# Kernel tuning notes

Hardware: AMD Instinct MI355X
Metric: run time of the kernel (lower is better)

Reference implementation:

```python
import jax, jax.numpy as jnp
import numpy as np

TOP_K = 8
SCALE = 2.5  # moe_router_scaling_factor
EPS = 1e-20


def setup_inputs() -> dict:
    key = jax.random.key(0)
    k1, k2 = jax.random.split(key)
    B, S, H, E = 4, 4096, 4096, 64
    hidden_states = jax.random.normal(k1, (B, S, H), dtype=jnp.float32)
    gate_weight = jax.random.normal(k2, (E, H), dtype=jnp.float32) * 0.02
    router_bias = jnp.zeros((E,), dtype=jnp.float32)
    return {"hidden_states": hidden_states, "gate_weight": gate_weight, "router_bias": router_bias}


def reference(hidden_states, gate_weight, router_bias):
    B, S, H = hidden_states.shape
    x = hidden_states.reshape(-1, H).astype(jnp.float32)  # [T, H]
    # need_fp32_gate: fp32 matmul against gate weight transpose -> [T, E]
    logits = jnp.einsum('th,eh->te', x, gate_weight.astype(jnp.float32))
    gate_prob = jax.nn.sigmoid(logits)
    biased = gate_prob + router_bias[None, :]
    # topk on bias-shifted probs; weights gathered from UNbiased probs
    _, indices = jax.lax.top_k(biased, TOP_K)                       # [T, K]
    topk_prob = jnp.take_along_axis(gate_prob, indices, axis=1)     # [T, K]
    weights = topk_prob / (jnp.sum(topk_prob, axis=-1, keepdims=True) + EPS)
    weights = weights * SCALE
    return weights, indices
```

## Files before the change

### kernel.cpp

```cpp
#include <hip/hip_runtime.h>
#include <cmath>


typedef float f32x4 __attribute__((ext_vector_type(4)));
typedef short s16x8 __attribute__((ext_vector_type(8)));
typedef unsigned int u32;
typedef u32 u32x4 __attribute__((ext_vector_type(4)));

#define E_DIM 64
#define KC 32
#define CH_BYTES 12288
#define NPART 4
#define HI_OFF (2u << 20)

union V16 { u32x4 u; s16x8 s; };

__device__ __forceinline__ unsigned short f2bf(float f) {
  unsigned u = __float_as_uint(f);
  u += 0x7fffu + ((u >> 16) & 1u);
  return (unsigned short)(u >> 16);
}
__device__ __forceinline__ float bf2f(unsigned short s) {
  return __uint_as_float(((unsigned)s) << 16);
}

__global__ __launch_bounds__(256) void split_w(
    const float* __restrict__ w, unsigned char* __restrict__ w3, int Hdim)
{
  const int kpr = Hdim >> 4;
  const int g = blockIdx.x * 256 + threadIdx.x;
  const int e = g / kpr;
  const int k0 = (g - e * kpr) * 16;
  if (e >= E_DIM) return;

  const float* src = w + (size_t)e * Hdim + k0;
  float f[16];
#pragma unroll
  for (int i = 0; i < 4; ++i) {
    float4 v = *(const float4*)(src + i * 4);
    f[i*4+0] = v.x; f[i*4+1] = v.y; f[i*4+2] = v.z; f[i*4+3] = v.w;
  }
  unsigned short hs[16], ms[16], ls[16];
#pragma unroll
  for (int i = 0; i < 16; ++i) {
    unsigned short h = f2bf(f[i]);
    float r1 = f[i] - bf2f(h);
    unsigned short m = f2bf(r1);
    float r2 = r1 - bf2f(m);
    hs[i] = h; ms[i] = m; ls[i] = f2bf(r2);
  }
  const int c  = k0 >> 5;
  const int n  = e >> 4;
  const int la = (e & 15) + (((k0 & 31) >> 3) << 4);
  unsigned char* base = w3 + (size_t)c * CH_BYTES + n * 1024;

#define STORE_SPLIT(arr, s)                                              \
  do {                                                                   \
    s16x8 pa, pb;                                                        \
    _Pragma("unroll")                                                    \
    for (int j = 0; j < 8; ++j) { pa[j] = (short)arr[j]; pb[j] = (short)arr[8+j]; } \
    *(s16x8*)(base + (s)*4096 + la * 16)        = pa;                    \
    *(s16x8*)(base + (s)*4096 + (la + 16) * 16) = pb;                    \
  } while (0)

  STORE_SPLIT(hs, 0);
  STORE_SPLIT(ms, 1);
  STORE_SPLIT(ls, 2);
#undef STORE_SPLIT
}

__global__ __launch_bounds__(256, 2) void router_mfma(
    const float* __restrict__ x, const unsigned char* __restrict__ w3,
    const float* __restrict__ bias, float* __restrict__ outw,
    float* __restrict__ outi, float* __restrict__ hi_p,
    float* __restrict__ lo_p, int T, int Hdim)
{
  const int tid  = threadIdx.x;
  const int wid  = tid >> 6;
  const int lane = tid & 63;
  const int lc   = lane & 15;
  const int lq   = lane >> 4;
  const int by   = blockIdx.y;
  const int nch  = Hdim / KC / gridDim.y;
  const int t0w  = blockIdx.x * 128 + wid * 32;

  const float* x0 = x + (size_t)(t0w + lc) * Hdim + (size_t)by * nch * KC + lq * 8;
  const float* x1 = x0 + (size_t)16 * Hdim;
  const unsigned char* wb = w3 + (size_t)by * nch * CH_BYTES + lane * 16;

  f32x4 acc[2][4];
  f32x4 sum_[2][4];
  f32x4 comp[2][4];
#pragma unroll
  for (int t = 0; t < 2; ++t)
#pragma unroll
    for (int n = 0; n < 4; ++n) {
      acc[t][n] = (f32x4){0,0,0,0};
      sum_[t][n] = (f32x4){0,0,0,0};
      comp[t][n] = (f32x4){0,0,0,0};
    }

#define LOADB(c, B)                                                          \
  do {                                                                       \
    const unsigned char* p_ = wb + (size_t)(c) * CH_BYTES;                   \
    _Pragma("unroll")                                                        \
    for (int s = 0; s < 3; ++s) {                                            \
      const unsigned char* ps_ = p_ + s * 4096;                              \
      _Pragma("unroll")                                                      \
      for (int n = 0; n < 4; ++n)                                            \
        B[s*4+n] = *(const s16x8*)(ps_ + n * 1024);                          \
    }                                                                        \
  } while (0)

#define LOADX(c, X)                                                          \
  do {                                                                       \
    X[0] = *(const float4*)(x0 + (size_t)(c) * KC);                          \
    X[1] = *(const float4*)(x0 + (size_t)(c) * KC + 4);                      \
    X[2] = *(const float4*)(x1 + (size_t)(c) * KC);                          \
    X[3] = *(const float4*)(x1 + (size_t)(c) * KC + 4);                      \
  } while (0)

#define SPLIT_PAIR(f0, f1, i, AHU, AMU, ALU)                                 \
  do {                                                                       \
    u32 u0_ = __float_as_uint(f0), u1_ = __float_as_uint(f1);                \
    u32 v0_ = u0_ + 0x8000u, v1_ = u1_ + 0x8000u;                            \
    AHU[i] = __builtin_amdgcn_perm(v1_, v0_, 0x07060302u);                   \
    float r0_ = (f0) - __uint_as_float(v0_ & 0xffff0000u);                   \
    float r1_ = (f1) - __uint_as_float(v1_ & 0xffff0000u);                   \
    u32 w0_ = __float_as_uint(r0_) + 0x8000u;                                \
    u32 w1_ = __float_as_uint(r1_) + 0x8000u;                                \
    AMU[i] = __builtin_amdgcn_perm(w1_, w0_, 0x07060302u);                   \
    float s0_ = r0_ - __uint_as_float(w0_ & 0xffff0000u);                    \
    float s1_ = r1_ - __uint_as_float(w1_ & 0xffff0000u);                    \
    u32 y0_ = __float_as_uint(s0_) + 0x8000u;                                \
    u32 y1_ = __float_as_uint(s1_) + 0x8000u;                                \
    ALU[i] = __builtin_amdgcn_perm(y1_, y0_, 0x07060302u);                   \
  } while (0)

#define COMPUTE(X, B)                                                        \
  do {                                                                       \
    _Pragma("unroll")                                                        \
    for (int t = 0; t < 2; ++t) {                                            \
      V16 ah_, am_, al_;                                                     \
      SPLIT_PAIR(X[t*2].x, X[t*2].y, 0, ah_.u, am_.u, al_.u);                \
      SPLIT_PAIR(X[t*2].z, X[t*2].w, 1, ah_.u, am_.u, al_.u);                \
      SPLIT_PAIR(X[t*2+1].x, X[t*2+1].y, 2, ah_.u, am_.u, al_.u);            \
      SPLIT_PAIR(X[t*2+1].z, X[t*2+1].w, 3, ah_.u, am_.u, al_.u);            \
      s16x8 ah = ah_.s, am = am_.s, al = al_.s;                              \
      __builtin_amdgcn_s_setprio(1);                                         \
      _Pragma("unroll")                                                      \
      for (int n = 0; n < 4; ++n) {                                          \
        acc[t][n] = __builtin_amdgcn_mfma_f32_16x16x32_bf16(ah, B[n],   acc[t][n], 0,0,0); \
        acc[t][n] = __builtin_amdgcn_mfma_f32_16x16x32_bf16(ah, B[4+n], acc[t][n], 0,0,0); \
        acc[t][n] = __builtin_amdgcn_mfma_f32_16x16x32_bf16(am, B[n],   acc[t][n], 0,0,0); \
        acc[t][n] = __builtin_amdgcn_mfma_f32_16x16x32_bf16(ah, B[8+n], acc[t][n], 0,0,0); \
        acc[t][n] = __builtin_amdgcn_mfma_f32_16x16x32_bf16(am, B[4+n], acc[t][n], 0,0,0); \
        acc[t][n] = __builtin_amdgcn_mfma_f32_16x16x32_bf16(al, B[n],   acc[t][n], 0,0,0); \
      }                                                                      \
      __builtin_amdgcn_s_setprio(0);                                         \
    }                                                                        \
  } while (0)

#define FOLD()                                                               \
  do {                                                                       \
    _Pragma("unroll")                                                        \
    for (int t = 0; t < 2; ++t)                                              \
      _Pragma("unroll")                                                      \
      for (int n = 0; n < 4; ++n)                                            \
        _Pragma("unroll")                                                    \
        for (int r = 0; r < 4; ++r) {                                        \
          float a_ = acc[t][n][r];                                           \
          float s_ = sum_[t][n][r];                                          \
          float t_ = s_ + a_;                                                \
          float z_ = t_ - s_;                                                \
          comp[t][n][r] += (s_ - (t_ - z_)) + (a_ - z_);                     \
          sum_[t][n][r] = t_;                                                \
          acc[t][n][r] = 0.f;                                                \
        }                                                                    \
  } while (0)

  float4 XA[4], XB[4];
  s16x8 BA[12], BB[12];

  LOADB(0, BA);
  LOADX(0, XA);

#pragma unroll 1
  for (int c = 0; c < nch; c += 2) {
    LOADB(c + 1, BB);
    LOADX(c + 1, XB);
    COMPUTE(XA, BA);
    if (c + 2 < nch) { LOADB(c + 2, BA); LOADX(c + 2, XA); }
    COMPUTE(XB, BB);
    if ((c & 2) == 2) FOLD();
  }
  FOLD();

  if (gridDim.y != 1) {
#pragma unroll
    for (int t = 0; t < 2; ++t)
#pragma unroll
      for (int n = 0; n < 4; ++n)
#pragma unroll
        for (int r = 0; r < 4; ++r) {
          const int tok = t0w + t * 16 + lq * 4 + r;
          const size_t o = ((size_t)by * T + tok) * E_DIM + n * 16 + lc;
          hi_p[o] = sum_[t][n][r];
          lo_p[o] = comp[t][n][r];
        }
    return;
  }

  float bias_v[4];
#pragma unroll
  for (int n = 0; n < 4; ++n) bias_v[n] = bias[n * 16 + lc];

#pragma unroll
  for (int t = 0; t < 2; ++t) {
    float pr[4][4], bi[4][4];
#pragma unroll
    for (int n = 0; n < 4; ++n)
#pragma unroll
      for (int r = 0; r < 4; ++r) {
        float logit = sum_[t][n][r] + comp[t][n][r];
        float p = 1.0f / (1.0f + expf(-logit));
        pr[n][r] = p;
        bi[n][r] = p + bias_v[n];
      }
#pragma unroll
    for (int r = 0; r < 4; ++r) {
      float v0 = bi[0][r], v1 = bi[1][r], v2 = bi[2][r], v3 = bi[3][r];
      float p0 = pr[0][r], p1 = pr[1][r], p2 = pr[2][r], p3 = pr[3][r];
      float sum = 0.f, selp = 0.f;
      int seli = 0;
#pragma unroll
      for (int k = 0; k < 8; ++k) {
        float bv = v0; int bn = 0; float bp = p0;
        if (v1 > bv) { bv = v1; bn = 1; bp = p1; }
        if (v2 > bv) { bv = v2; bn = 2; bp = p2; }
        if (v3 > bv) { bv = v3; bn = 3; bp = p3; }
        int be = bn * 16 + lc;
#pragma unroll
        for (int off = 8; off >= 1; off >>= 1) {
          float ov = __shfl_xor(bv, off);
          float op = __shfl_xor(bp, off);
          int   oe = __shfl_xor(be, off);
          if (ov > bv || (ov == bv && oe < be)) { bv = ov; bp = op; be = oe; }
        }
        sum += bp;
        if (lc == k) { selp = bp; seli = be; }
        if (lc == (be & 15)) {
          int gsel = be >> 4;
          if      (gsel == 0) v0 = -1e30f;
          else if (gsel == 1) v1 = -1e30f;
          else if (gsel == 2) v2 = -1e30f;
          else                v3 = -1e30f;
        }
      }
      if (lc < 8) {
        const int tok = t0w + t * 16 + lq * 4 + r;
        outw[(size_t)tok * 8 + lc] = selp * 2.5f / (sum + 1e-20f);
        outi[(size_t)tok * 8 + lc] = (float)seli;
      }
    }
  }
}

__global__ __launch_bounds__(256) void router_topk(
    const float* __restrict__ hi_p, const float* __restrict__ lo_p,
    const float* __restrict__ bias, float* __restrict__ outw,
    float* __restrict__ outi, int T)
{
  const int lane = threadIdx.x & 63;
  const int t = blockIdx.x * 4 + (threadIdx.x >> 6);
  if (t >= T) return;

  float s = 0.f, c = 0.f, losum = 0.f;
#pragma unroll
  for (int p = 0; p < NPART; ++p) {
    const size_t o = ((size_t)p * T + t) * E_DIM + lane;
    float a = hi_p[o];
    float tt = s + a;
    float z = tt - s;
    c += (s - (tt - z)) + (a - z);
    s = tt;
    losum += lo_p[o];
  }
  const float logit = s + (c + losum);

  const float prob = 1.0f / (1.0f + expf(-logit));
  float v = prob + bias[lane];

  float sum = 0.f, selw = 0.f;
  int seli = 0;
#pragma unroll
  for (int k = 0; k < 8; ++k) {
    float rv = v;
    int   ri = lane;
#pragma unroll
    for (int off = 32; off > 0; off >>= 1) {
      float ov = __shfl_xor(rv, off);
      int   oi = __shfl_xor(ri, off);
      if (ov > rv || (ov == rv && oi < ri)) { rv = ov; ri = oi; }
    }
    float pwin = __shfl(prob, ri);
    sum += pwin;
    if (lane == k)  { selw = pwin; seli = ri; }
    if (lane == ri) v = -INFINITY;
  }

  if (lane < 8) {
    float scale = 2.5f / (sum + 1e-20f);
    outw[(size_t)t * 8 + lane] = selw * scale;
    outi[(size_t)t * 8 + lane] = (float)seli;
  }
}

extern "C" void kernel_launch(void* const* d_in, const int* in_sizes, int n_in,
                              void* d_out, int out_size, void* d_ws, size_t ws_size,
                              hipStream_t stream) {
  const float* x    = (const float*)d_in[0];
  const float* w    = (const float*)d_in[1];
  const float* bias = (const float*)d_in[2];

  const int E    = in_sizes[2];
  const int Hdim = in_sizes[1] / E;
  const int T    = in_sizes[0] / Hdim;

  unsigned char* ws = (unsigned char*)d_ws;
  unsigned char* w3 = ws;
  float* hi_p = (float*)(ws + HI_OFF);
  float* lo_p = hi_p + (size_t)NPART * T * E_DIM;

  const size_t need = (size_t)HI_OFF + (size_t)2 * NPART * T * E_DIM * sizeof(float);
  const int nparts = (ws_size >= need) ? NPART : 1;

  const int nElemGroups = E * Hdim / 16;
  split_w<<<(nElemGroups + 255) / 256, 256, 0, stream>>>(w, w3, Hdim);

  float* outw = (float*)d_out;
  float* outi = outw + (size_t)T * 8;

  dim3 gridG(T / 128, nparts);
  router_mfma<<<gridG, 256, 0, stream>>>(x, w3, bias, outw, outi, hi_p, lo_p, T, Hdim);

  if (nparts != 1) {
    router_topk<<<(T + 3) / 4, 256, 0, stream>>>(hi_p, lo_p, bias, outw, outi, T);
  }
}
```

Before: 124.1 us.

## Use single-wave blocks and half-chunk B pipelining with scheduling barriers

Shrinks each block of the router GEMM kernel to one 64-lane wave covering 32 tokens, and raises the grid size to match. The main loop becomes a software pipeline: the B fragments are loaded in two halves (6 registers each instead of two 12-register buffers), X is prefetched two chunks ahead with four buffers, and sched_barrier fences interleave global loads with the MFMA groups. The aim is to cut register pressure and overlap memory latency with matrix work in this bandwidth-heavy fp32-split GEMM. In exchange it adds more blocks and drops the final FOLD, which assumes the chunk count is a multiple of four.

```diff
diff --git a/kernel.cpp b/kernel.cpp
--- a/kernel.cpp
+++ b/kernel.cpp
@@ -69,20 +69,18 @@
 #undef STORE_SPLIT
 }
 
-__global__ __launch_bounds__(256, 2) void router_mfma(
+__global__ __launch_bounds__(64, 2) void router_mfma(
     const float* __restrict__ x, const unsigned char* __restrict__ w3,
     const float* __restrict__ bias, float* __restrict__ outw,
     float* __restrict__ outi, float* __restrict__ hi_p,
     float* __restrict__ lo_p, int T, int Hdim)
 {
-  const int tid  = threadIdx.x;
-  const int wid  = tid >> 6;
-  const int lane = tid & 63;
+  const int lane = threadIdx.x;
   const int lc   = lane & 15;
   const int lq   = lane >> 4;
   const int by   = blockIdx.y;
   const int nch  = Hdim / KC / gridDim.y;
-  const int t0w  = blockIdx.x * 128 + wid * 32;
+  const int t0w  = blockIdx.x * 32;
 
   const float* x0 = x + (size_t)(t0w + lc) * Hdim + (size_t)by * nch * KC + lq * 8;
   const float* x1 = x0 + (size_t)16 * Hdim;
@@ -100,16 +98,16 @@
       comp[t][n] = (f32x4){0,0,0,0};
     }
 
-#define LOADB(c, B)                                                          \
-  do {                                                                       \
-    const unsigned char* p_ = wb + (size_t)(c) * CH_BYTES;                   \
+#define SB() __builtin_amdgcn_sched_barrier(0)
+
+#define LOADB_H(c, h, B)                                                     \
+  do {                                                                       \
+    const unsigned char* p_ = wb + (size_t)(c) * CH_BYTES + (h) * 2048;      \
     _Pragma("unroll")                                                        \
-    for (int s = 0; s < 3; ++s) {                                            \
-      const unsigned char* ps_ = p_ + s * 4096;                              \
+    for (int s = 0; s < 3; ++s)                                              \
       _Pragma("unroll")                                                      \
-      for (int n = 0; n < 4; ++n)                                            \
-        B[s*4+n] = *(const s16x8*)(ps_ + n * 1024);                          \
-    }                                                                        \
+      for (int j = 0; j < 2; ++j)                                            \
+        B[s*2+j] = *(const s16x8*)(p_ + s * 4096 + j * 1024);                \
   } while (0)
 
 #define LOADX(c, X)                                                          \
@@ -137,7 +135,7 @@
     ALU[i] = __builtin_amdgcn_perm(y1_, y0_, 0x07060302u);                   \
   } while (0)
 
-#define COMPUTE(X, B)                                                        \
+#define CONVERT(X)                                                           \
   do {                                                                       \
     _Pragma("unroll")                                                        \
     for (int t = 0; t < 2; ++t) {                                            \
@@ -146,19 +144,27 @@
       SPLIT_PAIR(X[t*2].z, X[t*2].w, 1, ah_.u, am_.u, al_.u);                \
       SPLIT_PAIR(X[t*2+1].x, X[t*2+1].y, 2, ah_.u, am_.u, al_.u);            \
       SPLIT_PAIR(X[t*2+1].z, X[t*2+1].w, 3, ah_.u, am_.u, al_.u);            \
-      s16x8 ah = ah_.s, am = am_.s, al = al_.s;                              \
-      __builtin_amdgcn_s_setprio(1);                                         \
+      Aah[t] = ah_.s; Aam[t] = am_.s; Aal[t] = al_.s;                        \
+    }                                                                        \
+  } while (0)
+
+#define COMPUTE_HALF(B, h)                                                   \
+  do {                                                                       \
+    __builtin_amdgcn_s_setprio(1);                                           \
+    _Pragma("unroll")                                                        \
+    for (int p = 0; p < 6; ++p)                                              \
       _Pragma("unroll")                                                      \
-      for (int n = 0; n < 4; ++n) {                                          \
-        acc[t][n] = __builtin_amdgcn_mfma_f32_16x16x32_bf16(ah, B[n],   acc[t][n], 0,0,0); \
-        acc[t][n] = __builtin_amdgcn_mfma_f32_16x16x32_bf16(ah, B[4+n], acc[t][n], 0,0,0); \
-        acc[t][n] = __builtin_amdgcn_mfma_f32_16x16x32_bf16(am, B[n],   acc[t][n], 0,0,0); \
-        acc[t][n] = __builtin_amdgcn_mfma_f32_16x16x32_bf16(ah, B[8+n], acc[t][n], 0,0,0); \
-        acc[t][n] = __builtin_amdgcn_mfma_f32_16x16x32_bf16(am, B[4+n], acc[t][n], 0,0,0); \
-        acc[t][n] = __builtin_amdgcn_mfma_f32_16x16x32_bf16(al, B[n],   acc[t][n], 0,0,0); \
-      }                                                                      \
-      __builtin_amdgcn_s_setprio(0);                                         \
-    }                                                                        \
+      for (int t = 0; t < 2; ++t)                                            \
+        _Pragma("unroll")                                                    \
+        for (int j = 0; j < 2; ++j) {                                        \
+          const s16x8 a_ = (p==0||p==2||p==5) ? Aah[t]                       \
+                         : (p==1||p==4)       ? Aam[t] : Aal[t];             \
+          const s16x8 b_ = (p==0||p==1||p==3) ? B[j]                         \
+                         : (p==2||p==4)       ? B[2+j] : B[4+j];             \
+          acc[t][2*(h)+j] =                                                  \
+            __builtin_amdgcn_mfma_f32_16x16x32_bf16(a_, b_, acc[t][2*(h)+j], 0,0,0); \
+        }                                                                    \
+    __builtin_amdgcn_s_setprio(0);                                           \
   } while (0)
 
 #define FOLD()                                                               \
@@ -179,22 +185,48 @@
         }                                                                    \
   } while (0)
 
-  float4 XA[4], XB[4];
-  s16x8 BA[12], BB[12];
-
-  LOADB(0, BA);
-  LOADX(0, XA);
+#define SUBITER(ca, XC0, XC1, XN0, XN1)                                      \
+  do {                                                                       \
+    const int cp2 = ((ca) + 2 < nch) ? (ca) + 2 : 0;                         \
+    const int cp3 = ((ca) + 3 < nch) ? (ca) + 3 : 0;                         \
+    LOADX(cp2, XN0);                                                         \
+    SB();                                                                    \
+    CONVERT(XC0);                                                            \
+    COMPUTE_HALF(B0, 0);                                                     \
+    SB();                                                                    \
+    LOADB_H((ca) + 1, 0, B0);                                                \
+    SB();                                                                    \
+    COMPUTE_HALF(B1, 1);                                                     \
+    SB();                                                                    \
+    LOADB_H((ca) + 1, 1, B1);                                                \
+    LOADX(cp3, XN1);                                                         \
+    SB();                                                                    \
+    CONVERT(XC1);                                                            \
+    COMPUTE_HALF(B0, 0);                                                     \
+    SB();                                                                    \
+    LOADB_H(cp2, 0, B0);                                                     \
+    SB();                                                                    \
+    COMPUTE_HALF(B1, 1);                                                     \
+    SB();                                                                    \
+    LOADB_H(cp2, 1, B1);                                                     \
+    SB();                                                                    \
+  } while (0)
+
+  float4 X0[4], X1[4], X2[4], X3[4];
+  s16x8 B0[6], B1[6];
+  s16x8 Aah[2], Aam[2], Aal[2];
+
+  LOADB_H(0, 0, B0);
+  LOADB_H(0, 1, B1);
+  LOADX(0, X0);
+  LOADX(1, X1);
 
 #pragma unroll 1
-  for (int c = 0; c < nch; c += 2) {
-    LOADB(c + 1, BB);
-    LOADX(c + 1, XB);
-    COMPUTE(XA, BA);
-    if (c + 2 < nch) { LOADB(c + 2, BA); LOADX(c + 2, XA); }
-    COMPUTE(XB, BB);
-    if ((c & 2) == 2) FOLD();
-  }
-  FOLD();
+  for (int c = 0; c < nch; c += 4) {
+    SUBITER(c,     X0, X1, X2, X3);
+    SUBITER(c + 2, X2, X3, X0, X1);
+    FOLD();
+  }
 
   if (gridDim.y != 1) {
 #pragma unroll
@@ -341,8 +373,8 @@
   float* outw = (float*)d_out;
   float* outi = outw + (size_t)T * 8;
 
-  dim3 gridG(T / 128, nparts);
-  router_mfma<<<gridG, 256, 0, stream>>>(x, w3, bias, outw, outi, hi_p, lo_p, T, Hdim);
+  dim3 gridG(T / 32, nparts);
+  router_mfma<<<gridG, 64, 0, stream>>>(x, w3, bias, outw, outi, hi_p, lo_p, T, Hdim);
 
   if (nparts != 1) {
     router_topk<<<(T + 3) / 4, 256, 0, stream>>>(hi_p, lo_p, bias, outw, outi, T);
```

Result: no change. 122.9 us (-1.0%).

## Stage split gate weights in LDS via direct global-to-LDS loads with double buffering

Applied to the files above, without the earlier changes.

Weight chunks are now loaded cooperatively by the whole block into a double-buffered LDS tile using global_load_lds, instead of each wave loading all weight fragments into registers. Each wave now handles 16 tokens rather than 32, so blocks cover 64 tokens and the grid doubles; occupancy hint rises to 3 blocks per CU. The aim is to cut redundant per-wave weight traffic and register pressure, and to overlap the next chunk's load with MFMA work. In exchange it adds block barriers on every chunk and LDS reads of B fragments, and the weights are reused across half as many tokens per wave.

```diff
diff --git a/kernel.cpp b/kernel.cpp
--- a/kernel.cpp
+++ b/kernel.cpp
@@ -69,12 +69,14 @@
 #undef STORE_SPLIT
 }
 
-__global__ __launch_bounds__(256, 2) void router_mfma(
+__global__ __launch_bounds__(256, 3) void router_mfma(
     const float* __restrict__ x, const unsigned char* __restrict__ w3,
     const float* __restrict__ bias, float* __restrict__ outw,
     float* __restrict__ outi, float* __restrict__ hi_p,
     float* __restrict__ lo_p, int T, int Hdim)
 {
+  __shared__ __align__(16) unsigned char lds[2][CH_BYTES];
+
   const int tid  = threadIdx.x;
   const int wid  = tid >> 6;
   const int lane = tid & 63;
@@ -82,42 +84,40 @@
   const int lq   = lane >> 4;
   const int by   = blockIdx.y;
   const int nch  = Hdim / KC / gridDim.y;
-  const int t0w  = blockIdx.x * 128 + wid * 32;
-
-  const float* x0 = x + (size_t)(t0w + lc) * Hdim + (size_t)by * nch * KC + lq * 8;
-  const float* x1 = x0 + (size_t)16 * Hdim;
-  const unsigned char* wb = w3 + (size_t)by * nch * CH_BYTES + lane * 16;
-
-  f32x4 acc[2][4];
-  f32x4 sum_[2][4];
-  f32x4 comp[2][4];
-#pragma unroll
-  for (int t = 0; t < 2; ++t)
-#pragma unroll
-    for (int n = 0; n < 4; ++n) {
-      acc[t][n] = (f32x4){0,0,0,0};
-      sum_[t][n] = (f32x4){0,0,0,0};
-      comp[t][n] = (f32x4){0,0,0,0};
-    }
-
-#define LOADB(c, B)                                                          \
-  do {                                                                       \
-    const unsigned char* p_ = wb + (size_t)(c) * CH_BYTES;                   \
+  const int t0   = blockIdx.x * 64;
+
+  const float* xp = x + (size_t)(t0 + wid * 16 + lc) * Hdim
+                      + (size_t)by * nch * KC + lq * 8;
+  const unsigned char* w3p = w3 + (size_t)by * nch * CH_BYTES;
+
+  f32x4 acc[4], sum_[4], comp[4];
+#pragma unroll
+  for (int n = 0; n < 4; ++n) {
+    acc[n] = (f32x4){0,0,0,0};
+    sum_[n] = (f32x4){0,0,0,0};
+    comp[n] = (f32x4){0,0,0,0};
+  }
+
+#define WAITV2() asm volatile("s_waitcnt vmcnt(2)" ::: "memory")
+#define WAITV0() asm volatile("s_waitcnt vmcnt(0)" ::: "memory")
+#define BAR()    __builtin_amdgcn_s_barrier()
+
+#define STAGE(c, b)                                                          \
+  do {                                                                       \
+    const unsigned char* gs = w3p + (size_t)(c) * CH_BYTES + tid * 16;       \
+    unsigned char* ld_ = &lds[b][0] + tid * 16;                              \
     _Pragma("unroll")                                                        \
-    for (int s = 0; s < 3; ++s) {                                            \
-      const unsigned char* ps_ = p_ + s * 4096;                              \
-      _Pragma("unroll")                                                      \
-      for (int n = 0; n < 4; ++n)                                            \
-        B[s*4+n] = *(const s16x8*)(ps_ + n * 1024);                          \
-    }                                                                        \
+    for (int i = 0; i < 3; ++i)                                              \
+      __builtin_amdgcn_global_load_lds(                                      \
+          (const __attribute__((address_space(1))) unsigned int*)(gs + i*4096), \
+          (__attribute__((address_space(3))) unsigned int*)(ld_ + i*4096),   \
+          16, 0, 0);                                                         \
   } while (0)
 
 #define LOADX(c, X)                                                          \
   do {                                                                       \
-    X[0] = *(const float4*)(x0 + (size_t)(c) * KC);                          \
-    X[1] = *(const float4*)(x0 + (size_t)(c) * KC + 4);                      \
-    X[2] = *(const float4*)(x1 + (size_t)(c) * KC);                          \
-    X[3] = *(const float4*)(x1 + (size_t)(c) * KC + 4);                      \
+    X[0] = *(const float4*)(xp + (size_t)(c) * KC);                          \
+    X[1] = *(const float4*)(xp + (size_t)(c) * KC + 4);                      \
   } while (0)
 
 #define SPLIT_PAIR(f0, f1, i, AHU, AMU, ALU)                                 \
@@ -137,77 +137,113 @@
     ALU[i] = __builtin_amdgcn_perm(y1_, y0_, 0x07060302u);                   \
   } while (0)
 
-#define COMPUTE(X, B)                                                        \
-  do {                                                                       \
+#define CONVERT(X)                                                           \
+  do {                                                                       \
+    V16 ah_, am_, al_;                                                       \
+    SPLIT_PAIR(X[0].x, X[0].y, 0, ah_.u, am_.u, al_.u);                      \
+    SPLIT_PAIR(X[0].z, X[0].w, 1, ah_.u, am_.u, al_.u);                      \
+    SPLIT_PAIR(X[1].x, X[1].y, 2, ah_.u, am_.u, al_.u);                      \
+    SPLIT_PAIR(X[1].z, X[1].w, 3, ah_.u, am_.u, al_.u);                      \
+    Aah = ah_.s; Aam = am_.s; Aal = al_.s;                                   \
+  } while (0)
+
+#define MFMA_ALL(b)                                                          \
+  do {                                                                       \
+    const unsigned char* B_ = &lds[b][0] + lane * 16;                        \
+    __builtin_amdgcn_s_setprio(1);                                           \
     _Pragma("unroll")                                                        \
-    for (int t = 0; t < 2; ++t) {                                            \
-      V16 ah_, am_, al_;                                                     \
-      SPLIT_PAIR(X[t*2].x, X[t*2].y, 0, ah_.u, am_.u, al_.u);                \
-      SPLIT_PAIR(X[t*2].z, X[t*2].w, 1, ah_.u, am_.u, al_.u);                \
-      SPLIT_PAIR(X[t*2+1].x, X[t*2+1].y, 2, ah_.u, am_.u, al_.u);            \
-      SPLIT_PAIR(X[t*2+1].z, X[t*2+1].w, 3, ah_.u, am_.u, al_.u);            \
-      s16x8 ah = ah_.s, am = am_.s, al = al_.s;                              \
-      __builtin_amdgcn_s_setprio(1);                                         \
+    for (int g = 0; g < 2; ++g) {                                            \
+      s16x8 bh0 = *(const s16x8*)(B_ + 0*4096 + (2*g)*1024);                 \
+      s16x8 bh1 = *(const s16x8*)(B_ + 0*4096 + (2*g+1)*1024);               \
+      s16x8 bm0 = *(const s16x8*)(B_ + 1*4096 + (2*g)*1024);                 \
+      s16x8 bm1 = *(const s16x8*)(B_ + 1*4096 + (2*g+1)*1024);               \
+      s16x8 bl0 = *(const s16x8*)(B_ + 2*4096 + (2*g)*1024);                 \
+      s16x8 bl1 = *(const s16x8*)(B_ + 2*4096 + (2*g+1)*1024);               \
+      acc[2*g]   = __builtin_amdgcn_mfma_f32_16x16x32_bf16(Aah, bh0, acc[2*g],   0,0,0); \
+      acc[2*g+1] = __builtin_amdgcn_mfma_f32_16x16x32_bf16(Aah, bh1, acc[2*g+1], 0,0,0); \
+      acc[2*g]   = __builtin_amdgcn_mfma_f32_16x16x32_bf16(Aah, bm0, acc[2*g],   0,0,0); \
+      acc[2*g+1] = __builtin_amdgcn_mfma_f32_16x16x32_bf16(Aah, bm1, acc[2*g+1], 0,0,0); \
+      acc[2*g]   = __builtin_amdgcn_mfma_f32_16x16x32_bf16(Aam, bh0, acc[2*g],   0,0,0); \
+      acc[2*g+1] = __builtin_amdgcn_mfma_f32_16x16x32_bf16(Aam, bh1, acc[2*g+1], 0,0,0); \
+      acc[2*g]   = __builtin_amdgcn_mfma_f32_16x16x32_bf16(Aah, bl0, acc[2*g],   0,0,0); \
+      acc[2*g+1] = __builtin_amdgcn_mfma_f32_16x16x32_bf16(Aah, bl1, acc[2*g+1], 0,0,0); \
+      acc[2*g]   = __builtin_amdgcn_mfma_f32_16x16x32_bf16(Aam, bm0, acc[2*g],   0,0,0); \
+      acc[2*g+1] = __builtin_amdgcn_mfma_f32_16x16x32_bf16(Aam, bm1, acc[2*g+1], 0,0,0); \
+      acc[2*g]   = __builtin_amdgcn_mfma_f32_16x16x32_bf16(Aal, bh0, acc[2*g],   0,0,0); \
+      acc[2*g+1] = __builtin_amdgcn_mfma_f32_16x16x32_bf16(Aal, bh1, acc[2*g+1], 0,0,0); \
+    }                                                                        \
+    __builtin_amdgcn_s_setprio(0);                                           \
+  } while (0)
+
+#define FOLD()                                                               \
+  do {                                                                       \
+    _Pragma("unroll")                                                        \
+    for (int n = 0; n < 4; ++n)                                              \
       _Pragma("unroll")                                                      \
-      for (int n = 0; n < 4; ++n) {                                          \
-        acc[t][n] = __builtin_amdgcn_mfma_f32_16x16x32_bf16(ah, B[n],   acc[t][n], 0,0,0); \
-        acc[t][n] = __builtin_amdgcn_mfma_f32_16x16x32_bf16(ah, B[4+n], acc[t][n], 0,0,0); \
-        acc[t][n] = __builtin_amdgcn_mfma_f32_16x16x32_bf16(am, B[n],   acc[t][n], 0,0,0); \
-        acc[t][n] = __builtin_amdgcn_mfma_f32_16x16x32_bf16(ah, B[8+n], acc[t][n], 0,0,0); \
-        acc[t][n] = __builtin_amdgcn_mfma_f32_16x16x32_bf16(am, B[4+n], acc[t][n], 0,0,0); \
-        acc[t][n] = __builtin_amdgcn_mfma_f32_16x16x32_bf16(al, B[n],   acc[t][n], 0,0,0); \
+      for (int r = 0; r < 4; ++r) {                                          \
+        float a_ = acc[n][r];                                                \
+        float s_ = sum_[n][r];                                               \
+        float t_ = s_ + a_;                                                  \
+        float z_ = t_ - s_;                                                  \
+        comp[n][r] += (s_ - (t_ - z_)) + (a_ - z_);                          \
+        sum_[n][r] = t_;                                                     \
+        acc[n][r] = 0.f;                                                     \
       }                                                                      \
-      __builtin_amdgcn_s_setprio(0);                                         \
-    }                                                                        \
-  } while (0)
-
-#define FOLD()                                                               \
-  do {                                                                       \
-    _Pragma("unroll")                                                        \
-    for (int t = 0; t < 2; ++t)                                              \
-      _Pragma("unroll")                                                      \
-      for (int n = 0; n < 4; ++n)                                            \
-        _Pragma("unroll")                                                    \
-        for (int r = 0; r < 4; ++r) {                                        \
-          float a_ = acc[t][n][r];                                           \
-          float s_ = sum_[t][n][r];                                          \
-          float t_ = s_ + a_;                                                \
-          float z_ = t_ - s_;                                                \
-          comp[t][n][r] += (s_ - (t_ - z_)) + (a_ - z_);                     \
-          sum_[t][n][r] = t_;                                                \
-          acc[t][n][r] = 0.f;                                                \
-        }                                                                    \
-  } while (0)
-
-  float4 XA[4], XB[4];
-  s16x8 BA[12], BB[12];
-
-  LOADB(0, BA);
-  LOADX(0, XA);
+  } while (0)
+
+#define ITER_FULL(c, k, XCUR, XN2)                                           \
+  do {                                                                       \
+    STAGE((c) + 1, ((k) + 1) & 1);                                           \
+    LOADX((c) + 2, XN2);                                                     \
+    CONVERT(XCUR);                                                           \
+    __builtin_amdgcn_sched_barrier(0);                                       \
+    MFMA_ALL((k) & 1);                                                       \
+    WAITV2();                                                                \
+    BAR();                                                                   \
+  } while (0)
+
+  float4 X0[2], X1[2], X2[2], X3[2];
+  s16x8 Aah, Aam, Aal;
+
+  STAGE(0, 0);
+  LOADX(0, X0);
+  LOADX(1, X1);
+  asm volatile("s_waitcnt vmcnt(4)" ::: "memory");
+  BAR();
 
 #pragma unroll 1
-  for (int c = 0; c < nch; c += 2) {
-    LOADB(c + 1, BB);
-    LOADX(c + 1, XB);
-    COMPUTE(XA, BA);
-    if (c + 2 < nch) { LOADB(c + 2, BA); LOADX(c + 2, XA); }
-    COMPUTE(XB, BB);
-    if ((c & 2) == 2) FOLD();
-  }
-  FOLD();
+  for (int c = 0; c + 4 < nch; c += 4) {
+    ITER_FULL(c + 0, 0, X0, X2);
+    ITER_FULL(c + 1, 1, X1, X3);
+    ITER_FULL(c + 2, 2, X2, X0);
+    ITER_FULL(c + 3, 3, X3, X1);
+    FOLD();
+  }
+  {
+    const int c = nch - 4;
+    ITER_FULL(c + 0, 0, X0, X2);
+    ITER_FULL(c + 1, 1, X1, X3);
+    STAGE(c + 3, 1);
+    CONVERT(X2);
+    __builtin_amdgcn_sched_barrier(0);
+    MFMA_ALL(0);
+    WAITV0();
+    BAR();
+    CONVERT(X3);
+    MFMA_ALL(1);
+    FOLD();
+  }
 
   if (gridDim.y != 1) {
 #pragma unroll
-    for (int t = 0; t < 2; ++t)
-#pragma unroll
-      for (int n = 0; n < 4; ++n)
-#pragma unroll
-        for (int r = 0; r < 4; ++r) {
-          const int tok = t0w + t * 16 + lq * 4 + r;
-          const size_t o = ((size_t)by * T + tok) * E_DIM + n * 16 + lc;
-          hi_p[o] = sum_[t][n][r];
-          lo_p[o] = comp[t][n][r];
-        }
+    for (int n = 0; n < 4; ++n)
+#pragma unroll
+      for (int r = 0; r < 4; ++r) {
+        const int tok = t0 + wid * 16 + lq * 4 + r;
+        const size_t o = ((size_t)by * T + tok) * E_DIM + n * 16 + lc;
+        hi_p[o] = sum_[n][r];
+        lo_p[o] = comp[n][r];
+      }
     return;
   }
 
@@ -215,53 +251,50 @@
 #pragma unroll
   for (int n = 0; n < 4; ++n) bias_v[n] = bias[n * 16 + lc];
 
-#pragma unroll
-  for (int t = 0; t < 2; ++t) {
-    float pr[4][4], bi[4][4];
-#pragma unroll
-    for (int n = 0; n < 4; ++n)
-#pragma unroll
-      for (int r = 0; r < 4; ++r) {
-        float logit = sum_[t][n][r] + comp[t][n][r];
-        float p = 1.0f / (1.0f + expf(-logit));
-        pr[n][r] = p;
-        bi[n][r] = p + bias_v[n];
+  float pr[4][4], bi[4][4];
+#pragma unroll
+  for (int n = 0; n < 4; ++n)
+#pragma unroll
+    for (int r = 0; r < 4; ++r) {
+      float logit = sum_[n][r] + comp[n][r];
+      float p = 1.0f / (1.0f + expf(-logit));
+      pr[n][r] = p;
+      bi[n][r] = p + bias_v[n];
+    }
+#pragma unroll
+  for (int r = 0; r < 4; ++r) {
+    float v0 = bi[0][r], v1 = bi[1][r], v2 = bi[2][r], v3 = bi[3][r];
+    float p0 = pr[0][r], p1 = pr[1][r], p2 = pr[2][r], p3 = pr[3][r];
+    float sum = 0.f, selp = 0.f;
+    int seli = 0;
+#pragma unroll
+    for (int k = 0; k < 8; ++k) {
+      float bv = v0; int bn = 0; float bp = p0;
+      if (v1 > bv) { bv = v1; bn = 1; bp = p1; }
+      if (v2 > bv) { bv = v2; bn = 2; bp = p2; }
+      if (v3 > bv) { bv = v3; bn = 3; bp = p3; }
+      int be = bn * 16 + lc;
+#pragma unroll
+      for (int off = 8; off >= 1; off >>= 1) {
+        float ov = __shfl_xor(bv, off);
+        float op = __shfl_xor(bp, off);
+        int   oe = __shfl_xor(be, off);
+        if (ov > bv || (ov == bv && oe < be)) { bv = ov; bp = op; be = oe; }
       }
-#pragma unroll
-    for (int r = 0; r < 4; ++r) {
-      float v0 = bi[0][r], v1 = bi[1][r], v2 = bi[2][r], v3 = bi[3][r];
-      float p0 = pr[0][r], p1 = pr[1][r], p2 = pr[2][r], p3 = pr[3][r];
-      float sum = 0.f, selp = 0.f;
-      int seli = 0;
-#pragma unroll
-      for (int k = 0; k < 8; ++k) {
-        float bv = v0; int bn = 0; float bp = p0;
-        if (v1 > bv) { bv = v1; bn = 1; bp = p1; }
-        if (v2 > bv) { bv = v2; bn = 2; bp = p2; }
-        if (v3 > bv) { bv = v3; bn = 3; bp = p3; }
-        int be = bn * 16 + lc;
-#pragma unroll
-        for (int off = 8; off >= 1; off >>= 1) {
-          float ov = __shfl_xor(bv, off);
-          float op = __shfl_xor(bp, off);
-          int   oe = __shfl_xor(be, off);
-          if (ov > bv || (ov == bv && oe < be)) { bv = ov; bp = op; be = oe; }
-        }
-        sum += bp;
-        if (lc == k) { selp = bp; seli = be; }
-        if (lc == (be & 15)) {
-          int gsel = be >> 4;
-          if      (gsel == 0) v0 = -1e30f;
-          else if (gsel == 1) v1 = -1e30f;
-          else if (gsel == 2) v2 = -1e30f;
-          else                v3 = -1e30f;
-        }
+      sum += bp;
+      if (lc == k) { selp = bp; seli = be; }
+      if (lc == (be & 15)) {
+        int gsel = be >> 4;
+        if      (gsel == 0) v0 = -1e30f;
+        else if (gsel == 1) v1 = -1e30f;
+        else if (gsel == 2) v2 = -1e30f;
+        else                v3 = -1e30f;
       }
-      if (lc < 8) {
-        const int tok = t0w + t * 16 + lq * 4 + r;
-        outw[(size_t)tok * 8 + lc] = selp * 2.5f / (sum + 1e-20f);
-        outi[(size_t)tok * 8 + lc] = (float)seli;
-      }
+    }
+    if (lc < 8) {
+      const int tok = t0 + wid * 16 + lq * 4 + r;
+      outw[(size_t)tok * 8 + lc] = selp * 2.5f / (sum + 1e-20f);
+      outi[(size_t)tok * 8 + lc] = (float)seli;
     }
   }
 }
@@ -341,7 +374,7 @@
   float* outw = (float*)d_out;
   float* outi = outw + (size_t)T * 8;
 
-  dim3 gridG(T / 128, nparts);
+  dim3 gridG(T / 64, nparts);
   router_mfma<<<gridG, 256, 0, stream>>>(x, w3, bias, outw, outi, hi_p, lo_p, T, Hdim);
 
   if (nparts != 1) {
```

After: 112.3 us. -9.5%, faster.
